# Kernel tuning notes

Hardware: AMD Instinct MI355X
Metric: run time of the kernel (lower is better)

Reference implementation:

```python
import jax, jax.numpy as jnp
import numpy as np

B, S, D = 4, 2048, 1024

def setup_inputs() -> dict:
    key = jax.random.key(0)
    kv, kk, kq, kw = jax.random.split(key, 4)
    scale = 1.0 / np.sqrt(D)
    v = jax.random.normal(kv, (B, S, D), dtype=jnp.float32)
    k = jax.random.normal(kk, (B, S, D), dtype=jnp.float32)
    q = jax.random.normal(kq, (B, S, D), dtype=jnp.float32)
    wi = jax.random.normal(kw, (D, D), dtype=jnp.float32) * scale
    mask = jnp.tril(jnp.ones((S, S), dtype=bool))[None, :, :]  # causal [1,S,S]
    return {"v": v, "k": k, "q": q, "wi": wi, "mask": mask}

def reference(v, k, q, wi, mask):
    # project q, k, v with the shared weight wi
    q = q @ wi
    k = k @ wi
    v = v @ wi
    # scaled dot-product scores [B,S,S]
    scores = jnp.einsum('bqd,bkd->bqk', q, k) / jnp.sqrt(jnp.asarray(q.shape[-1], q.dtype))
    scores = jnp.where(mask, scores, jnp.asarray(-1e10, scores.dtype))
    attn = jax.nn.softmax(scores, axis=-1)
    # residual: q + attn @ v
    return q + jnp.einsum('bqk,bkd->bqd', attn, v)
```

## Files before the change

### kernel.cpp

```cpp
#include <hip/hip_runtime.h>
#include <hip/hip_bf16.h>

typedef __hip_bfloat16 bf16;
typedef short bf16x8 __attribute__((ext_vector_type(8)));
typedef float f32x4 __attribute__((ext_vector_type(4)));

#define HT 16384

__device__ __forceinline__ void gload16(const void* g, void* l) {
    __builtin_amdgcn_global_load_lds(
        (const __attribute__((address_space(1))) void*)g,
        (__attribute__((address_space(3))) void*)l, 16, 0, 0);
}

__device__ __forceinline__ void stage_half(char* lds, const bf16* src, int ld,
                                           int rowbase, int k0, int slotIdx,
                                           int tid)
{
    char* dst = lds + (size_t)slotIdx * HT + tid * 16;
    const int sub = tid >> 3;
    const int cb  = ((tid & 7) ^ (sub & 7)) << 4;
    #pragma unroll
    for (int p = 0; p < 2; ++p) {
        const int row = p * 64 + sub;
        const char* g = (const char*)(src + (size_t)(rowbase + row) * ld + k0) + cb;
        gload16(g, dst + p * 8192);
    }
}

__device__ __forceinline__ void stage_q(char* lds, const bf16* src, int ld,
                                        int rowbase, int k0, int slotIdx,
                                        int tid)
{
    char* dst = lds + (size_t)slotIdx * HT + tid * 16;
    #pragma unroll
    for (int p = 0; p < 4; ++p) {
        const int s = p * 256 + tid;
        const int row = s >> 3;
        const int cb = ((s & 7) ^ (row & 7)) << 4;
        const char* g = (const char*)(src + (size_t)(rowbase + row) * ld + k0) + cb;
        gload16(g, dst + p * 4096);
    }
}

__device__ __forceinline__ bf16x8 ldsfrag(const char* lds, int slotIdx,
                                          int row, int ks, int cb0)
{
    return *(const bf16x8*)(lds + (size_t)slotIdx * HT
                            + row * 128 + (cb0 ^ (ks << 6)));
}

__device__ __forceinline__ float bf2f(short s) {
    union { float f; unsigned u; } c;
    c.u = ((unsigned)(unsigned short)s) << 16;
    return c.f;
}

#define MF8(n0)                                                               \
    _Pragma("unroll") for (int m = 0; m < 4; ++m)                             \
    _Pragma("unroll") for (int dn = 0; dn < 2; ++dn)                          \
    _Pragma("unroll") for (int ks = 0; ks < 2; ++ks)                          \
        acc[m][(n0)+dn] = __builtin_amdgcn_mfma_f32_16x16x32_bf16(            \
            af[m][ks], bv[(n0)+dn][ks], acc[m][(n0)+dn], 0, 0, 0);

#define GEMM256_BODY(A_, lda_, B_, ldb_, brow_, bcol_)                        \
    f32x4 acc[4][4] = {};                                                     \
    bf16x8 af[4][2], bv[4][2];                                                \
    stage_half(lds, A_, lda_, brow_,       0, 0, tid);                        \
    stage_half(lds, A_, lda_, brow_ + 128, 0, 1, tid);                        \
    stage_half(lds, B_, ldb_, bcol_,       0, 6, tid);                        \
    stage_half(lds, A_, lda_, brow_,      64, 2, tid);                        \
    stage_half(lds, A_, lda_, brow_ + 128,64, 3, tid);                        \
    stage_half(lds, B_, ldb_, bcol_,     64, 7, tid);                         \
    asm volatile("s_waitcnt vmcnt(6)" ::: "memory");                          \
    __builtin_amdgcn_s_barrier();                                             \
    for (int t = 0; t < 16; ++t) {                                            \
        const int aslot = (t % 3) * 2 + hA;                                   \
        const int bslot = 6 + (t & 1);                                        \
        const int a2    = ((t + 2) % 3) * 2;                                  \
        const int k2    = min(t + 2, 15) << 6;                                \
        _Pragma("unroll") for (int m = 0; m < 4; ++m)                         \
        _Pragma("unroll") for (int ks = 0; ks < 2; ++ks)                      \
            af[m][ks] = ldsfrag(lds, aslot, rA + m * 16 + fr, ks, cb0);       \
        _Pragma("unroll") for (int n = 0; n < 4; ++n)                         \
        _Pragma("unroll") for (int ks = 0; ks < 2; ++ks)                      \
            bv[n][ks] = ldsfrag(lds, bslot, rB + n * 16 + fr, ks, cb0);       \
        stage_half(lds, A_, lda_, brow_,       k2, a2,     tid);              \
        stage_half(lds, A_, lda_, brow_ + 128, k2, a2 + 1, tid);              \
        __builtin_amdgcn_s_barrier();                                         \
        __builtin_amdgcn_s_setprio(1);                                        \
        MF8(0)                                                                \
        __builtin_amdgcn_s_setprio(0);                                        \
        __builtin_amdgcn_s_barrier();                                         \
        stage_half(lds, B_, ldb_, bcol_, k2, bslot, tid);                     \
        __builtin_amdgcn_s_barrier();                                         \
        __builtin_amdgcn_s_setprio(1);                                        \
        MF8(2)                                                                \
        __builtin_amdgcn_s_setprio(0);                                        \
        asm volatile("s_waitcnt vmcnt(6)" ::: "memory");                      \
        __builtin_amdgcn_s_barrier();                                         \
    }

template<int MODE>
__launch_bounds__(512, 2)
__global__ void gemm_a256(const bf16* __restrict__ A, const bf16* __restrict__ B,
                          bf16* __restrict__ Cb, float* __restrict__ Cf)
{
    extern __shared__ char lds[];
    const int gx = gridDim.x;
    const int nwg = gx * gridDim.y;
    const int chunk = nwg >> 3;
    const int orig = blockIdx.y * gx + blockIdx.x;
    const int wk2 = (orig & 7) * chunk + (orig >> 3);
    const int bi = wk2 / gx, bj = wk2 % gx;
    const int brow = bi * 256, bcol = bj * 128;

    const int tid  = threadIdx.x;
    const int lane = tid & 63;
    const int w    = tid >> 6;
    const int wm   = w >> 1, wn = w & 1;
    const int fr   = lane & 15, fq = lane >> 4;
    const int cb0  = ((fr & 7) ^ fq) << 4;
    const int hA   = wm >> 1;
    const int rA   = (wm & 1) * 64;
    const int rB   = wn * 64;

    GEMM256_BODY(A, 1024, B, 1024, brow, bcol)

    #pragma unroll
    for (int mf = 0; mf < 4; ++mf) {
        const int r0 = brow + wm * 64 + mf * 16 + fq * 4;
        #pragma unroll
        for (int nf = 0; nf < 4; ++nf) {
            const int c = bcol + wn * 64 + nf * 16 + fr;
            #pragma unroll
            for (int j = 0; j < 4; ++j) {
                if (MODE == 0)
                    Cb[(size_t)(r0 + j) * 1024 + c] =
                        __float2bfloat16(acc[mf][nf][j]);
                else
                    Cf[(size_t)(r0 + j) * 1024 + c] = acc[mf][nf][j];
            }
        }
    }
}

__launch_bounds__(512, 1)
__global__ void scores8(const bf16* __restrict__ qG, const bf16* __restrict__ kb,
                        bf16* __restrict__ P)
{
    extern __shared__ char lds[];
    const int orig = blockIdx.y * 8 + blockIdx.x;
    const int wk2 = (orig & 7) * 18 + (orig >> 3);
    const int bz = wk2 / 36;
    const int j  = wk2 % 36;
    int bi = (int)((__fsqrt_rn(8.0f * j + 1.0f) - 1.0f) * 0.5f);
    while ((bi + 1) * (bi + 2) / 2 <= j) ++bi;
    while (bi * (bi + 1) / 2 > j) --bi;
    const int bj = j - bi * (bi + 1) / 2;
    const int brow = bi * 256, bcol = bj * 256;
    const bf16* A = qG + (size_t)bz * 2048 * 1024;
    const bf16* B = kb + (size_t)bz * 2048 * 1024;
    bf16* Cp = P + (size_t)bz * 2048 * 2048;

    const int tid  = threadIdx.x;
    const int lane = tid & 63;
    const int w    = tid >> 6;
    const int wm   = w >> 2;
    const int wn   = w & 3;
    const int bh   = wn >> 1;
    const int rBl  = (wn & 1) * 64;
    const int fr   = lane & 15, fq = lane >> 4;
    const int cb0  = ((fr & 7) ^ fq) << 4;

    f32x4 acc[8][4] = {};
    bf16x8 af0[4][2], af1[4][2], bv0[2][2], bv1[2][2];

#define AS(t,h) ((((t) % 3) * 2) + (h))
#define BS(t,h) (6 + (((t) & 1) * 2) + (h))

    stage_half(lds, A, 1024, brow,       0, AS(0,0), tid);
    stage_half(lds, A, 1024, brow + 128, 0, AS(0,1), tid);
    stage_half(lds, B, 1024, bcol,       0, BS(0,0), tid);
    stage_half(lds, B, 1024, bcol + 128, 0, BS(0,1), tid);
    stage_half(lds, A, 1024, brow,      64, AS(1,0), tid);
    stage_half(lds, A, 1024, brow + 128,64, AS(1,1), tid);
    stage_half(lds, B, 1024, bcol,     64, BS(1,0), tid);
    asm volatile("s_waitcnt vmcnt(6)" ::: "memory");
    __builtin_amdgcn_s_barrier();

#define MFQ(MH, NH, AF, BV)                                                   \
    _Pragma("unroll") for (int m = 0; m < 4; ++m)                             \
    _Pragma("unroll") for (int n = 0; n < 2; ++n)                             \
    _Pragma("unroll") for (int ks = 0; ks < 2; ++ks)                          \
        acc[(MH)*4+m][(NH)*2+n] = __builtin_amdgcn_mfma_f32_16x16x32_bf16(    \
            AF[m][ks], BV[n][ks], acc[(MH)*4+m][(NH)*2+n], 0, 0, 0);

    for (int t = 0; t < 16; ++t) {
        const int kN  = min(t + 1, 15) << 6;
        const int kNN = min(t + 2, 15) << 6;
        const int as  = AS(t, wm);
        const int bs2 = BS(t, bh);

        #pragma unroll
        for (int m = 0; m < 4; ++m)
            #pragma unroll
            for (int ks = 0; ks < 2; ++ks)
                af0[m][ks] = ldsfrag(lds, as, m * 16 + fr, ks, cb0);
        #pragma unroll
        for (int n = 0; n < 2; ++n)
            #pragma unroll
            for (int ks = 0; ks < 2; ++ks)
                bv0[n][ks] = ldsfrag(lds, bs2, rBl + n * 16 + fr, ks, cb0);
        stage_half(lds, B, 1024, bcol + 128, kN, BS(t + 1, 1), tid);
        __builtin_amdgcn_s_barrier();
        __builtin_amdgcn_s_setprio(1);
        MFQ(0, 0, af0, bv0)
        __builtin_amdgcn_s_setprio(0);
        __builtin_amdgcn_s_barrier();

        #pragma unroll
        for (int m = 0; m < 4; ++m)
            #pragma unroll
            for (int ks = 0; ks < 2; ++ks)
                af1[m][ks] = ldsfrag(lds, as, 64 + m * 16 + fr, ks, cb0);
        stage_half(lds, A, 1024, brow, kNN, AS(t + 2, 0), tid);
        __builtin_amdgcn_s_barrier();
        __builtin_amdgcn_s_setprio(1);
        MFQ(1, 0, af1, bv0)
        __builtin_amdgcn_s_setprio(0);
        __builtin_amdgcn_s_barrier();

        #pragma unroll
        for (int n = 0; n < 2; ++n)
            #pragma unroll
            for (int ks = 0; ks < 2; ++ks)
                bv1[n][ks] = ldsfrag(lds, bs2, rBl + 32 + n * 16 + fr, ks, cb0);
        stage_half(lds, A, 1024, brow + 128, kNN, AS(t + 2, 1), tid);
        __builtin_amdgcn_s_barrier();
        __builtin_amdgcn_s_setprio(1);
        MFQ(1, 1, af1, bv1)
        __builtin_amdgcn_s_setprio(0);
        __builtin_amdgcn_s_barrier();

        stage_half(lds, B, 1024, bcol, kNN, BS(t + 2, 0), tid);
        __builtin_amdgcn_s_barrier();
        __builtin_amdgcn_s_setprio(1);
        MFQ(0, 1, af0, bv1)
        __builtin_amdgcn_s_setprio(0);
        asm volatile("s_waitcnt vmcnt(6)" ::: "memory");
        __builtin_amdgcn_s_barrier();
    }
#undef MFQ
#undef AS
#undef BS

    #pragma unroll
    for (int mf = 0; mf < 8; ++mf) {
        const int r0 = brow + wm * 128 + mf * 16 + fq * 4;
        #pragma unroll
        for (int nf = 0; nf < 4; ++nf) {
            const int c = bcol + wn * 64 + nf * 16 + fr;
            #pragma unroll
            for (int jj = 0; jj < 4; ++jj)
                Cp[(size_t)(r0 + jj) * 2048 + c] =
                    __float2bfloat16(acc[mf][nf][jj] * 0.03125f);
        }
    }
}

__device__ __forceinline__ void tile128pv(char* lds, const bf16* A, const bf16* B,
                                          bf16* Cb, const bf16* Res,
                                          int lda, int ldb, int ldcb,
                                          int brow, int bcol, int NT, int tid)
{
    const int lane = tid & 63;
    const int w    = tid >> 6;
    const int wm   = w >> 1, wn = w & 1;
    const int fr   = lane & 15, fq = lane >> 4;
    const int cb0  = ((fr & 7) ^ fq) << 4;

    f32x4 acc[4][4] = {};
    bf16x8 af[4][2], bv[4][2];

    stage_q(lds, A, lda, brow, 0,  0, tid);
    stage_q(lds, B, ldb, bcol, 0,  3, tid);
    stage_q(lds, A, lda, brow, 64, 1, tid);
    stage_q(lds, B, ldb, bcol, 64, 4, tid);
    asm volatile("s_waitcnt vmcnt(8)" ::: "memory");
    __builtin_amdgcn_s_barrier();

    for (int t = 0; t < NT; ++t) {
        const int aslot = t % 3, bslot = 3 + (t & 1);
        const int k2 = min(t + 2, NT - 1) << 6;

        #pragma unroll
        for (int m = 0; m < 4; ++m)
            #pragma unroll
            for (int ks = 0; ks < 2; ++ks)
                af[m][ks] = ldsfrag(lds, aslot, wm * 64 + m * 16 + fr, ks, cb0);
        #pragma unroll
        for (int n = 0; n < 4; ++n)
            #pragma unroll
            for (int ks = 0; ks < 2; ++ks)
                bv[n][ks] = ldsfrag(lds, bslot, wn * 64 + n * 16 + fr, ks, cb0);
        stage_q(lds, A, lda, brow, k2, (t + 2) % 3, tid);
        __builtin_amdgcn_s_barrier();
        __builtin_amdgcn_s_setprio(1);
        #pragma unroll
        for (int m = 0; m < 4; ++m)
            #pragma unroll
            for (int n = 0; n < 2; ++n)
                #pragma unroll
                for (int ks = 0; ks < 2; ++ks)
                    acc[m][n] = __builtin_amdgcn_mfma_f32_16x16x32_bf16(
                        af[m][ks], bv[n][ks], acc[m][n], 0, 0, 0);
        __builtin_amdgcn_s_setprio(0);
        __builtin_amdgcn_s_barrier();

        stage_q(lds, B, ldb, bcol, k2, bslot, tid);
        __builtin_amdgcn_s_barrier();
        __builtin_amdgcn_s_setprio(1);
        #pragma unroll
        for (int m = 0; m < 4; ++m)
            #pragma unroll
            for (int n = 2; n < 4; ++n)
                #pragma unroll
                for (int ks = 0; ks < 2; ++ks)
                    acc[m][n] = __builtin_amdgcn_mfma_f32_16x16x32_bf16(
                        af[m][ks], bv[n][ks], acc[m][n], 0, 0, 0);
        __builtin_amdgcn_s_setprio(0);
        asm volatile("s_waitcnt vmcnt(8)" ::: "memory");
        __builtin_amdgcn_s_barrier();
    }

    #pragma unroll
    for (int mf = 0; mf < 4; ++mf) {
        const int r0 = brow + wm * 64 + mf * 16 + fq * 4;
        #pragma unroll
        for (int nf = 0; nf < 4; ++nf) {
            const int c = bcol + wn * 64 + nf * 16 + fr;
            #pragma unroll
            for (int j = 0; j < 4; ++j)
                Cb[(size_t)(r0 + j) * ldcb + c] = __float2bfloat16(
                    acc[mf][nf][j] +
                    __bfloat162float(Res[(size_t)(r0 + j) * ldcb + c]));
        }
    }
}

__launch_bounds__(256, 2)
__global__ void pv128(const bf16* __restrict__ P, const bf16* __restrict__ vT,
                      const bf16* __restrict__ qb, bf16* __restrict__ Y)
{
    extern __shared__ char lds[];
    const int x  = blockIdx.x;
    const int u  = x & 255;
    const int bs = u & 7;
    const int bj = (u >> 3) & 7;
    const int bz = u >> 6;
    const int bi = (x >> 8) ? (15 - bs) : bs;

    tile128pv(lds,
              P + (size_t)bz * 2048 * 2048,
              vT + (size_t)bz * 1024 * 2048,
              Y + (size_t)bz * 2048 * 1024,
              qb + (size_t)bz * 2048 * 1024,
              2048, 2048, 1024,
              bi * 128, bj * 128, 2 * (bi + 1), threadIdx.x);
}

__global__ void convert_qk_w(const float* __restrict__ q, const float* __restrict__ k,
                             const float* __restrict__ wi,
                             bf16* __restrict__ qb, bf16* __restrict__ kb,
                             bf16* __restrict__ Wb)
{
    const int N8 = 8192 * 1024 / 8;
    const int W8 = 1024 * 1024 / 8;
    const int total = 2 * N8 + W8;
    for (int i = blockIdx.x * 256 + threadIdx.x; i < total; i += gridDim.x * 256) {
        const float4* s;
        bf16* dst;
        int j;
        if (i < N8)            { s = (const float4*)q;  dst = qb; j = i; }
        else if (i < 2 * N8)   { s = (const float4*)k;  dst = kb; j = i - N8; }
        else                   { s = (const float4*)wi; dst = Wb; j = i - 2 * N8; }
        float4 a = s[2 * j], b = s[2 * j + 1];
        float vals[8] = {a.x, a.y, a.z, a.w, b.x, b.y, b.z, b.w};
        union { short h[8]; bf16x8 v8; } o;
        #pragma unroll
        for (int e = 0; e < 8; ++e) {
            bf16 hh = __float2bfloat16(vals[e]);
            o.h[e] = *(short*)&hh;
        }
        ((bf16x8*)dst)[j] = o.v8;
    }
}

__global__ void transpose_vwi(const float* __restrict__ v,
                              const float* __restrict__ wi,
                              bf16* __restrict__ vT, bf16* __restrict__ Wt)
{
    __shared__ float t[32][33];
    const int z = blockIdx.z;
    const int lx = threadIdx.x & 31, ly = threadIdx.x >> 5;
    if (z < 4) {
        const int d0 = blockIdx.x * 32, s0 = blockIdx.y * 32;
        const float* src = v + (size_t)z * 2048 * 1024;
        bf16* dst = vT + (size_t)z * 1024 * 2048;
        for (int i = ly; i < 32; i += 8)
            t[i][lx] = src[(size_t)(s0 + i) * 1024 + d0 + lx];
        __syncthreads();
        for (int i = ly; i < 32; i += 8)
            dst[(size_t)(d0 + i) * 2048 + s0 + lx] = __float2bfloat16(t[lx][i]);
    } else {
        if (blockIdx.y >= 32) return;
        const int n0 = blockIdx.x * 32, k0 = blockIdx.y * 32;
        for (int i = ly; i < 32; i += 8)
            t[i][lx] = wi[(size_t)(k0 + i) * 1024 + n0 + lx];
        __syncthreads();
        for (int i = ly; i < 32; i += 8)
            Wt[(size_t)(n0 + i) * 1024 + k0 + lx] = __float2bfloat16(t[lx][i]);
    }
}

__launch_bounds__(256)
__global__ void softmax_rows(bf16* __restrict__ P)
{
    const int wid = threadIdx.x >> 6, lane = threadIdx.x & 63;
    const int r = blockIdx.x * 4 + wid, b = blockIdx.y;
    bf16* row = P + ((size_t)b * 2048 + r) * 2048;
    const int nv  = r + 1;
    const int rup = (r & ~127) + 128;

    float vals[4][8];
    float m = -1e30f;
    #pragma unroll
    for (int c = 0; c < 4; ++c) {
        const int k0 = c * 512 + lane * 8;
        if (k0 < rup) {
            bf16x8 x = *(const bf16x8*)(row + k0);
            #pragma unroll
            for (int j = 0; j < 8; ++j) {
                float f = (k0 + j < nv) ? bf2f(x[j]) : -1e30f;
                vals[c][j] = f;
                m = fmaxf(m, f);
            }
        } else {
            #pragma unroll
            for (int j = 0; j < 8; ++j) vals[c][j] = -1e30f;
        }
    }
    #pragma unroll
    for (int o = 32; o; o >>= 1) m = fmaxf(m, __shfl_xor(m, o));

    float sum = 0.f;
    #pragma unroll
    for (int c = 0; c < 4; ++c)
        #pragma unroll
        for (int j = 0; j < 8; ++j) {
            float e = __expf(vals[c][j] - m);
            vals[c][j] = e;
            sum += e;
        }
    #pragma unroll
    for (int o = 32; o; o >>= 1) sum += __shfl_xor(sum, o);
    const float inv = 1.0f / sum;

    #pragma unroll
    for (int c = 0; c < 4; ++c) {
        const int k0 = c * 512 + lane * 8;
        if (k0 < rup) {
            union { short h[8]; bf16x8 v8; } o;
            #pragma unroll
            for (int j = 0; j < 8; ++j) {
                bf16 hh = __float2bfloat16(vals[c][j] * inv);
                o.h[j] = *(short*)&hh;
            }
            *(bf16x8*)(row + k0) = o.v8;
        }
    }
}

extern "C" void kernel_launch(void* const* d_in, const int* in_sizes, int n_in,
                              void* d_out, int out_size, void* d_ws, size_t ws_size,
                              hipStream_t stream)
{
    const float* v  = (const float*)d_in[0];
    const float* k  = (const float*)d_in[1];
    const float* q  = (const float*)d_in[2];
    const float* wi = (const float*)d_in[3];
    float* out = (float*)d_out;

    char* ws = (char*)d_ws;
    const size_t MB = 1u << 20;
    bf16* Wb = (bf16*)(ws);
    bf16* Wt = (bf16*)(ws + 2 * MB);
    bf16* G  = (bf16*)(ws + 4 * MB);
    bf16* qb = (bf16*)(ws + 6 * MB);
    bf16* kb = (bf16*)(ws + 22 * MB);
    bf16* vT = (bf16*)(ws + 38 * MB);
    bf16* qG = (bf16*)(ws + 54 * MB);
    bf16* Y  = (bf16*)(ws + 70 * MB);
    bf16* P  = (bf16*)(ws + 86 * MB);

    (void)hipFuncSetAttribute((const void*)gemm_a256<0>,
            hipFuncAttributeMaxDynamicSharedMemorySize, 131072);
    (void)hipFuncSetAttribute((const void*)gemm_a256<2>,
            hipFuncAttributeMaxDynamicSharedMemorySize, 131072);
    (void)hipFuncSetAttribute((const void*)scores8,
            hipFuncAttributeMaxDynamicSharedMemorySize, 163840);
    (void)hipFuncSetAttribute((const void*)pv128,
            hipFuncAttributeMaxDynamicSharedMemorySize, 81920);

    convert_qk_w<<<2048, 256, 0, stream>>>(q, k, wi, qb, kb, Wb);
    transpose_vwi<<<dim3(32, 64, 5), 256, 0, stream>>>(v, wi, vT, Wt);

    gemm_a256<0><<<dim3(8, 4), 512, 131072, stream>>>(Wb, Wb, G, nullptr);

    gemm_a256<0><<<dim3(8, 32), 512, 131072, stream>>>(qb, G, qG, nullptr);

    scores8<<<dim3(8, 18), 512, 163840, stream>>>(qG, kb, P);

    softmax_rows<<<dim3(512, 4), 256, 0, stream>>>(P);

    pv128<<<dim3(512), 256, 81920, stream>>>(P, vT, qb, Y);

    gemm_a256<2><<<dim3(8, 32), 512, 131072, stream>>>(Y, Wt, nullptr, out);
}
```

Before: 164.9 us.

## Fuse Gram, qG, scores and softmax into one cooperative persistent kernel

Merges the W·Wᵀ GEMM, the q·G projection, the causal score GEMM and the row softmax into a single cooperative kernel of 144 workgroups that separates phases with grid-wide syncs. The projection GEMMs now use the same 256x256 eight-phase tile routine as the score kernel. The conversion and transpose prep kernels are also merged into one launch. The aim is to remove launch gaps and tail effects between small dependent kernels. In exchange it adds grid-sync costs, leaves some workgroups idle in the early GEMM phases (16 and 128 of 144 tiles), and depends on cooperative launch co-residency.

```diff
diff --git a/kernel.cpp b/kernel.cpp
--- a/kernel.cpp
+++ b/kernel.cpp
@@ -1,5 +1,8 @@
 #include <hip/hip_runtime.h>
 #include <hip/hip_bf16.h>
+#include <hip/hip_cooperative_groups.h>
+
+namespace cg = cooperative_groups;
 
 typedef __hip_bfloat16 bf16;
 typedef short bf16x8 __attribute__((ext_vector_type(8)));
@@ -56,6 +59,318 @@
     return c.f;
 }
 
+__device__ __forceinline__ void tile256_8ph(char* lds,
+                                            const bf16* __restrict__ A,
+                                            const bf16* __restrict__ B,
+                                            bf16* __restrict__ C, int ldc,
+                                            int brow, int bcol, float scale,
+                                            int tid)
+{
+    const int lane = tid & 63;
+    const int w    = tid >> 6;
+    const int wm   = w >> 2;
+    const int wn   = w & 3;
+    const int bh   = wn >> 1;
+    const int rBl  = (wn & 1) * 64;
+    const int fr   = lane & 15, fq = lane >> 4;
+    const int cb0  = ((fr & 7) ^ fq) << 4;
+
+    f32x4 acc[8][4] = {};
+    bf16x8 af0[4][2], af1[4][2], bv0[2][2], bv1[2][2];
+
+#define AS(t,h) ((((t) % 3) * 2) + (h))
+#define BS(t,h) (6 + (((t) & 1) * 2) + (h))
+
+    stage_half(lds, A, 1024, brow,       0, AS(0,0), tid);
+    stage_half(lds, A, 1024, brow + 128, 0, AS(0,1), tid);
+    stage_half(lds, B, 1024, bcol,       0, BS(0,0), tid);
+    stage_half(lds, B, 1024, bcol + 128, 0, BS(0,1), tid);
+    stage_half(lds, A, 1024, brow,      64, AS(1,0), tid);
+    stage_half(lds, A, 1024, brow + 128,64, AS(1,1), tid);
+    stage_half(lds, B, 1024, bcol,     64, BS(1,0), tid);
+    asm volatile("s_waitcnt vmcnt(6)" ::: "memory");
+    __builtin_amdgcn_s_barrier();
+
+#define MFQ(MH, NH, AF, BV)                                                   \
+    _Pragma("unroll") for (int m = 0; m < 4; ++m)                             \
+    _Pragma("unroll") for (int n = 0; n < 2; ++n)                             \
+    _Pragma("unroll") for (int ks = 0; ks < 2; ++ks)                          \
+        acc[(MH)*4+m][(NH)*2+n] = __builtin_amdgcn_mfma_f32_16x16x32_bf16(    \
+            AF[m][ks], BV[n][ks], acc[(MH)*4+m][(NH)*2+n], 0, 0, 0);
+
+    for (int t = 0; t < 16; ++t) {
+        const int kN  = min(t + 1, 15) << 6;
+        const int kNN = min(t + 2, 15) << 6;
+        const int as  = AS(t, wm);
+        const int bs2 = BS(t, bh);
+
+        #pragma unroll
+        for (int m = 0; m < 4; ++m)
+            #pragma unroll
+            for (int ks = 0; ks < 2; ++ks)
+                af0[m][ks] = ldsfrag(lds, as, m * 16 + fr, ks, cb0);
+        #pragma unroll
+        for (int n = 0; n < 2; ++n)
+            #pragma unroll
+            for (int ks = 0; ks < 2; ++ks)
+                bv0[n][ks] = ldsfrag(lds, bs2, rBl + n * 16 + fr, ks, cb0);
+        stage_half(lds, B, 1024, bcol + 128, kN, BS(t + 1, 1), tid);
+        __builtin_amdgcn_s_barrier();
+        __builtin_amdgcn_s_setprio(1);
+        MFQ(0, 0, af0, bv0)
+        __builtin_amdgcn_s_setprio(0);
+        __builtin_amdgcn_s_barrier();
+
+        #pragma unroll
+        for (int m = 0; m < 4; ++m)
+            #pragma unroll
+            for (int ks = 0; ks < 2; ++ks)
+                af1[m][ks] = ldsfrag(lds, as, 64 + m * 16 + fr, ks, cb0);
+        stage_half(lds, A, 1024, brow, kNN, AS(t + 2, 0), tid);
+        __builtin_amdgcn_s_barrier();
+        __builtin_amdgcn_s_setprio(1);
+        MFQ(1, 0, af1, bv0)
+        __builtin_amdgcn_s_setprio(0);
+        __builtin_amdgcn_s_barrier();
+
+        #pragma unroll
+        for (int n = 0; n < 2; ++n)
+            #pragma unroll
+            for (int ks = 0; ks < 2; ++ks)
+                bv1[n][ks] = ldsfrag(lds, bs2, rBl + 32 + n * 16 + fr, ks, cb0);
+        stage_half(lds, A, 1024, brow + 128, kNN, AS(t + 2, 1), tid);
+        __builtin_amdgcn_s_barrier();
+        __builtin_amdgcn_s_setprio(1);
+        MFQ(1, 1, af1, bv1)
+        __builtin_amdgcn_s_setprio(0);
+        __builtin_amdgcn_s_barrier();
+
+        stage_half(lds, B, 1024, bcol, kNN, BS(t + 2, 0), tid);
+        __builtin_amdgcn_s_barrier();
+        __builtin_amdgcn_s_setprio(1);
+        MFQ(0, 1, af0, bv1)
+        __builtin_amdgcn_s_setprio(0);
+        asm volatile("s_waitcnt vmcnt(6)" ::: "memory");
+        __builtin_amdgcn_s_barrier();
+    }
+#undef MFQ
+#undef AS
+#undef BS
+
+    #pragma unroll
+    for (int mf = 0; mf < 8; ++mf) {
+        const int r0 = brow + wm * 128 + mf * 16 + fq * 4;
+        #pragma unroll
+        for (int nf = 0; nf < 4; ++nf) {
+            const int c = bcol + wn * 64 + nf * 16 + fr;
+            #pragma unroll
+            for (int jj = 0; jj < 4; ++jj)
+                C[(size_t)(r0 + jj) * ldc + c] =
+                    __float2bfloat16(acc[mf][nf][jj] * scale);
+        }
+    }
+    asm volatile("s_waitcnt vmcnt(0)" ::: "memory");
+    __builtin_amdgcn_s_barrier();
+}
+
+__launch_bounds__(512, 1)
+__global__ void attn_mega(const bf16* __restrict__ Wb,
+                          const bf16* __restrict__ qb,
+                          const bf16* __restrict__ kb,
+                          bf16* __restrict__ G, bf16* __restrict__ qG,
+                          bf16* __restrict__ P)
+{
+    extern __shared__ char lds[];
+    cg::grid_group grid = cg::this_grid();
+    const int orig = blockIdx.x;
+    const int wk2 = (orig & 7) * 18 + (orig >> 3);
+    const int tid = threadIdx.x;
+
+    if (wk2 < 16)
+        tile256_8ph(lds, Wb, Wb, G, 1024,
+                    (wk2 >> 2) * 256, (wk2 & 3) * 256, 1.0f, tid);
+    grid.sync();
+
+    if (wk2 < 128)
+        tile256_8ph(lds, qb, G, qG, 1024,
+                    (wk2 >> 2) * 256, (wk2 & 3) * 256, 1.0f, tid);
+    grid.sync();
+
+    {
+        const int bz = wk2 / 36;
+        const int j  = wk2 % 36;
+        int bi = (int)((__fsqrt_rn(8.0f * j + 1.0f) - 1.0f) * 0.5f);
+        while ((bi + 1) * (bi + 2) / 2 <= j) ++bi;
+        while (bi * (bi + 1) / 2 > j) --bi;
+        const int bj = j - bi * (bi + 1) / 2;
+        tile256_8ph(lds,
+                    qG + (size_t)bz * 2048 * 1024,
+                    kb + (size_t)bz * 2048 * 1024,
+                    P + (size_t)bz * 2048 * 2048, 2048,
+                    bi * 256, bj * 256, 0.03125f, tid);
+    }
+    grid.sync();
+
+    {
+        const int w = tid >> 6, lane = tid & 63;
+        for (int row = orig * 8 + w; row < 8192; row += 144 * 8) {
+            const int b = row >> 11, r = row & 2047;
+            bf16* rp = P + ((size_t)b * 2048 + r) * 2048;
+            const int nv  = r + 1;
+            const int rup = (r & ~127) + 128;
+
+            float vals[4][8];
+            float m = -1e30f;
+            #pragma unroll
+            for (int c = 0; c < 4; ++c) {
+                const int k0 = c * 512 + lane * 8;
+                if (k0 < rup) {
+                    bf16x8 x = *(const bf16x8*)(rp + k0);
+                    #pragma unroll
+                    for (int j = 0; j < 8; ++j) {
+                        float f = (k0 + j < nv) ? bf2f(x[j]) : -1e30f;
+                        vals[c][j] = f;
+                        m = fmaxf(m, f);
+                    }
+                } else {
+                    #pragma unroll
+                    for (int j = 0; j < 8; ++j) vals[c][j] = -1e30f;
+                }
+            }
+            #pragma unroll
+            for (int o = 32; o; o >>= 1) m = fmaxf(m, __shfl_xor(m, o));
+
+            float sum = 0.f;
+            #pragma unroll
+            for (int c = 0; c < 4; ++c)
+                #pragma unroll
+                for (int j = 0; j < 8; ++j) {
+                    float e = __expf(vals[c][j] - m);
+                    vals[c][j] = e;
+                    sum += e;
+                }
+            #pragma unroll
+            for (int o = 32; o; o >>= 1) sum += __shfl_xor(sum, o);
+            const float inv = 1.0f / sum;
+
+            #pragma unroll
+            for (int c = 0; c < 4; ++c) {
+                const int k0 = c * 512 + lane * 8;
+                if (k0 < rup) {
+                    union { short h[8]; bf16x8 v8; } o;
+                    #pragma unroll
+                    for (int j = 0; j < 8; ++j) {
+                        bf16 hh = __float2bfloat16(vals[c][j] * inv);
+                        o.h[j] = *(short*)&hh;
+                    }
+                    *(bf16x8*)(rp + k0) = o.v8;
+                }
+            }
+        }
+    }
+}
+
+__device__ __forceinline__ void tile128pv(char* lds, const bf16* A, const bf16* B,
+                                          bf16* Cb, const bf16* Res,
+                                          int lda, int ldb, int ldcb,
+                                          int brow, int bcol, int NT, int tid)
+{
+    const int lane = tid & 63;
+    const int w    = tid >> 6;
+    const int wm   = w >> 1, wn = w & 1;
+    const int fr   = lane & 15, fq = lane >> 4;
+    const int cb0  = ((fr & 7) ^ fq) << 4;
+
+    f32x4 acc[4][4] = {};
+    bf16x8 af[4][2], bv[4][2];
+
+    stage_q(lds, A, lda, brow, 0,  0, tid);
+    stage_q(lds, B, ldb, bcol, 0,  3, tid);
+    stage_q(lds, A, lda, brow, 64, 1, tid);
+    stage_q(lds, B, ldb, bcol, 64, 4, tid);
+    asm volatile("s_waitcnt vmcnt(8)" ::: "memory");
+    __builtin_amdgcn_s_barrier();
+
+    for (int t = 0; t < NT; ++t) {
+        const int aslot = t % 3, bslot = 3 + (t & 1);
+        const int k2 = min(t + 2, NT - 1) << 6;
+
+        #pragma unroll
+        for (int m = 0; m < 4; ++m)
+            #pragma unroll
+            for (int ks = 0; ks < 2; ++ks)
+                af[m][ks] = ldsfrag(lds, aslot, wm * 64 + m * 16 + fr, ks, cb0);
+        #pragma unroll
+        for (int n = 0; n < 4; ++n)
+            #pragma unroll
+            for (int ks = 0; ks < 2; ++ks)
+                bv[n][ks] = ldsfrag(lds, bslot, wn * 64 + n * 16 + fr, ks, cb0);
+        stage_q(lds, A, lda, brow, k2, (t + 2) % 3, tid);
+        __builtin_amdgcn_s_barrier();
+        __builtin_amdgcn_s_setprio(1);
+        #pragma unroll
+        for (int m = 0; m < 4; ++m)
+            #pragma unroll
+            for (int n = 0; n < 2; ++n)
+                #pragma unroll
+                for (int ks = 0; ks < 2; ++ks)
+                    acc[m][n] = __builtin_amdgcn_mfma_f32_16x16x32_bf16(
+                        af[m][ks], bv[n][ks], acc[m][n], 0, 0, 0);
+        __builtin_amdgcn_s_setprio(0);
+        __builtin_amdgcn_s_barrier();
+
+        stage_q(lds, B, ldb, bcol, k2, bslot, tid);
+        __builtin_amdgcn_s_barrier();
+        __builtin_amdgcn_s_setprio(1);
+        #pragma unroll
+        for (int m = 0; m < 4; ++m)
+            #pragma unroll
+            for (int n = 2; n < 4; ++n)
+                #pragma unroll
+                for (int ks = 0; ks < 2; ++ks)
+                    acc[m][n] = __builtin_amdgcn_mfma_f32_16x16x32_bf16(
+                        af[m][ks], bv[n][ks], acc[m][n], 0, 0, 0);
+        __builtin_amdgcn_s_setprio(0);
+        asm volatile("s_waitcnt vmcnt(8)" ::: "memory");
+        __builtin_amdgcn_s_barrier();
+    }
+
+    #pragma unroll
+    for (int mf = 0; mf < 4; ++mf) {
+        const int r0 = brow + wm * 64 + mf * 16 + fq * 4;
+        #pragma unroll
+        for (int nf = 0; nf < 4; ++nf) {
+            const int c = bcol + wn * 64 + nf * 16 + fr;
+            #pragma unroll
+            for (int j = 0; j < 4; ++j)
+                Cb[(size_t)(r0 + j) * ldcb + c] = __float2bfloat16(
+                    acc[mf][nf][j] +
+                    __bfloat162float(Res[(size_t)(r0 + j) * ldcb + c]));
+        }
+    }
+}
+
+__launch_bounds__(256, 2)
+__global__ void pv128(const bf16* __restrict__ P, const bf16* __restrict__ vT,
+                      const bf16* __restrict__ qb, bf16* __restrict__ Y)
+{
+    extern __shared__ char lds[];
+    const int x  = blockIdx.x;
+    const int u  = x & 255;
+    const int bs = u & 7;
+    const int bj = (u >> 3) & 7;
+    const int bz = u >> 6;
+    const int bi = (x >> 8) ? (15 - bs) : bs;
+
+    tile128pv(lds,
+              P + (size_t)bz * 2048 * 2048,
+              vT + (size_t)bz * 1024 * 2048,
+              Y + (size_t)bz * 2048 * 1024,
+              qb + (size_t)bz * 2048 * 1024,
+              2048, 2048, 1024,
+              bi * 128, bj * 128, 2 * (bi + 1), threadIdx.x);
+}
+
 #define MF8(n0)                                                               \
     _Pragma("unroll") for (int m = 0; m < 4; ++m)                             \
     _Pragma("unroll") for (int dn = 0; dn < 2; ++dn)                          \
@@ -63,48 +378,9 @@
         acc[m][(n0)+dn] = __builtin_amdgcn_mfma_f32_16x16x32_bf16(            \
             af[m][ks], bv[(n0)+dn][ks], acc[m][(n0)+dn], 0, 0, 0);
 
-#define GEMM256_BODY(A_, lda_, B_, ldb_, brow_, bcol_)                        \
-    f32x4 acc[4][4] = {};                                                     \
-    bf16x8 af[4][2], bv[4][2];                                                \
-    stage_half(lds, A_, lda_, brow_,       0, 0, tid);                        \
-    stage_half(lds, A_, lda_, brow_ + 128, 0, 1, tid);                        \
-    stage_half(lds, B_, ldb_, bcol_,       0, 6, tid);                        \
-    stage_half(lds, A_, lda_, brow_,      64, 2, tid);                        \
-    stage_half(lds, A_, lda_, brow_ + 128,64, 3, tid);                        \
-    stage_half(lds, B_, ldb_, bcol_,     64, 7, tid);                         \
-    asm volatile("s_waitcnt vmcnt(6)" ::: "memory");                          \
-    __builtin_amdgcn_s_barrier();                                             \
-    for (int t = 0; t < 16; ++t) {                                            \
-        const int aslot = (t % 3) * 2 + hA;                                   \
-        const int bslot = 6 + (t & 1);                                        \
-        const int a2    = ((t + 2) % 3) * 2;                                  \
-        const int k2    = min(t + 2, 15) << 6;                                \
-        _Pragma("unroll") for (int m = 0; m < 4; ++m)                         \
-        _Pragma("unroll") for (int ks = 0; ks < 2; ++ks)                      \
-            af[m][ks] = ldsfrag(lds, aslot, rA + m * 16 + fr, ks, cb0);       \
-        _Pragma("unroll") for (int n = 0; n < 4; ++n)                         \
-        _Pragma("unroll") for (int ks = 0; ks < 2; ++ks)                      \
-            bv[n][ks] = ldsfrag(lds, bslot, rB + n * 16 + fr, ks, cb0);       \
-        stage_half(lds, A_, lda_, brow_,       k2, a2,     tid);              \
-        stage_half(lds, A_, lda_, brow_ + 128, k2, a2 + 1, tid);              \
-        __builtin_amdgcn_s_barrier();                                         \
-        __builtin_amdgcn_s_setprio(1);                                        \
-        MF8(0)                                                                \
-        __builtin_amdgcn_s_setprio(0);                                        \
-        __builtin_amdgcn_s_barrier();                                         \
-        stage_half(lds, B_, ldb_, bcol_, k2, bslot, tid);                     \
-        __builtin_amdgcn_s_barrier();                                         \
-        __builtin_amdgcn_s_setprio(1);                                        \
-        MF8(2)                                                                \
-        __builtin_amdgcn_s_setprio(0);                                        \
-        asm volatile("s_waitcnt vmcnt(6)" ::: "memory");                      \
-        __builtin_amdgcn_s_barrier();                                         \
-    }
-
-template<int MODE>
 __launch_bounds__(512, 2)
-__global__ void gemm_a256(const bf16* __restrict__ A, const bf16* __restrict__ B,
-                          bf16* __restrict__ Cb, float* __restrict__ Cf)
+__global__ void final_gemm(const bf16* __restrict__ A, const bf16* __restrict__ B,
+                           float* __restrict__ Cf)
 {
     extern __shared__ char lds[];
     const int gx = gridDim.x;
@@ -125,7 +401,50 @@
     const int rA   = (wm & 1) * 64;
     const int rB   = wn * 64;
 
-    GEMM256_BODY(A, 1024, B, 1024, brow, bcol)
+    f32x4 acc[4][4] = {};
+    bf16x8 af[4][2], bv[4][2];
+
+    stage_half(lds, A, 1024, brow,       0, 0, tid);
+    stage_half(lds, A, 1024, brow + 128, 0, 1, tid);
+    stage_half(lds, B, 1024, bcol,       0, 6, tid);
+    stage_half(lds, A, 1024, brow,      64, 2, tid);
+    stage_half(lds, A, 1024, brow + 128,64, 3, tid);
+    stage_half(lds, B, 1024, bcol,     64, 7, tid);
+    asm volatile("s_waitcnt vmcnt(6)" ::: "memory");
+    __builtin_amdgcn_s_barrier();
+
+    for (int t = 0; t < 16; ++t) {
+        const int aslot = (t % 3) * 2 + hA;
+        const int bslot = 6 + (t & 1);
+        const int a2    = ((t + 2) % 3) * 2;
+        const int k2    = min(t + 2, 15) << 6;
+
+        #pragma unroll
+        for (int m = 0; m < 4; ++m)
+            #pragma unroll
+            for (int ks = 0; ks < 2; ++ks)
+                af[m][ks] = ldsfrag(lds, aslot, rA + m * 16 + fr, ks, cb0);
+        #pragma unroll
+        for (int n = 0; n < 4; ++n)
+            #pragma unroll
+            for (int ks = 0; ks < 2; ++ks)
+                bv[n][ks] = ldsfrag(lds, bslot, rB + n * 16 + fr, ks, cb0);
+        stage_half(lds, A, 1024, brow,       k2, a2,     tid);
+        stage_half(lds, A, 1024, brow + 128, k2, a2 + 1, tid);
+        __builtin_amdgcn_s_barrier();
+        __builtin_amdgcn_s_setprio(1);
+        MF8(0)
+        __builtin_amdgcn_s_setprio(0);
+        __builtin_amdgcn_s_barrier();
+
+        stage_half(lds, B, 1024, bcol, k2, bslot, tid);
+        __builtin_amdgcn_s_barrier();
+        __builtin_amdgcn_s_setprio(1);
+        MF8(2)
+        __builtin_amdgcn_s_setprio(0);
+        asm volatile("s_waitcnt vmcnt(6)" ::: "memory");
+        __builtin_amdgcn_s_barrier();
+    }
 
     #pragma unroll
     for (int mf = 0; mf < 4; ++mf) {
@@ -134,278 +453,24 @@
         for (int nf = 0; nf < 4; ++nf) {
             const int c = bcol + wn * 64 + nf * 16 + fr;
             #pragma unroll
-            for (int j = 0; j < 4; ++j) {
-                if (MODE == 0)
-                    Cb[(size_t)(r0 + j) * 1024 + c] =
-                        __float2bfloat16(acc[mf][nf][j]);
-                else
-                    Cf[(size_t)(r0 + j) * 1024 + c] = acc[mf][nf][j];
-            }
+            for (int j = 0; j < 4; ++j)
+                Cf[(size_t)(r0 + j) * 1024 + c] = acc[mf][nf][j];
         }
     }
 }
 
-__launch_bounds__(512, 1)
-__global__ void scores8(const bf16* __restrict__ qG, const bf16* __restrict__ kb,
-                        bf16* __restrict__ P)
-{
-    extern __shared__ char lds[];
-    const int orig = blockIdx.y * 8 + blockIdx.x;
-    const int wk2 = (orig & 7) * 18 + (orig >> 3);
-    const int bz = wk2 / 36;
-    const int j  = wk2 % 36;
-    int bi = (int)((__fsqrt_rn(8.0f * j + 1.0f) - 1.0f) * 0.5f);
-    while ((bi + 1) * (bi + 2) / 2 <= j) ++bi;
-    while (bi * (bi + 1) / 2 > j) --bi;
-    const int bj = j - bi * (bi + 1) / 2;
-    const int brow = bi * 256, bcol = bj * 256;
-    const bf16* A = qG + (size_t)bz * 2048 * 1024;
-    const bf16* B = kb + (size_t)bz * 2048 * 1024;
-    bf16* Cp = P + (size_t)bz * 2048 * 2048;
-
-    const int tid  = threadIdx.x;
-    const int lane = tid & 63;
-    const int w    = tid >> 6;
-    const int wm   = w >> 2;
-    const int wn   = w & 3;
-    const int bh   = wn >> 1;
-    const int rBl  = (wn & 1) * 64;
-    const int fr   = lane & 15, fq = lane >> 4;
-    const int cb0  = ((fr & 7) ^ fq) << 4;
-
-    f32x4 acc[8][4] = {};
-    bf16x8 af0[4][2], af1[4][2], bv0[2][2], bv1[2][2];
-
-#define AS(t,h) ((((t) % 3) * 2) + (h))
-#define BS(t,h) (6 + (((t) & 1) * 2) + (h))
-
-    stage_half(lds, A, 1024, brow,       0, AS(0,0), tid);
-    stage_half(lds, A, 1024, brow + 128, 0, AS(0,1), tid);
-    stage_half(lds, B, 1024, bcol,       0, BS(0,0), tid);
-    stage_half(lds, B, 1024, bcol + 128, 0, BS(0,1), tid);
-    stage_half(lds, A, 1024, brow,      64, AS(1,0), tid);
-    stage_half(lds, A, 1024, brow + 128,64, AS(1,1), tid);
-    stage_half(lds, B, 1024, bcol,     64, BS(1,0), tid);
-    asm volatile("s_waitcnt vmcnt(6)" ::: "memory");
-    __builtin_amdgcn_s_barrier();
-
-#define MFQ(MH, NH, AF, BV)                                                   \
-    _Pragma("unroll") for (int m = 0; m < 4; ++m)                             \
-    _Pragma("unroll") for (int n = 0; n < 2; ++n)                             \
-    _Pragma("unroll") for (int ks = 0; ks < 2; ++ks)                          \
-        acc[(MH)*4+m][(NH)*2+n] = __builtin_amdgcn_mfma_f32_16x16x32_bf16(    \
-            AF[m][ks], BV[n][ks], acc[(MH)*4+m][(NH)*2+n], 0, 0, 0);
-
-    for (int t = 0; t < 16; ++t) {
-        const int kN  = min(t + 1, 15) << 6;
-        const int kNN = min(t + 2, 15) << 6;
-        const int as  = AS(t, wm);
-        const int bs2 = BS(t, bh);
-
-        #pragma unroll
-        for (int m = 0; m < 4; ++m)
-            #pragma unroll
-            for (int ks = 0; ks < 2; ++ks)
-                af0[m][ks] = ldsfrag(lds, as, m * 16 + fr, ks, cb0);
-        #pragma unroll
-        for (int n = 0; n < 2; ++n)
-            #pragma unroll
-            for (int ks = 0; ks < 2; ++ks)
-                bv0[n][ks] = ldsfrag(lds, bs2, rBl + n * 16 + fr, ks, cb0);
-        stage_half(lds, B, 1024, bcol + 128, kN, BS(t + 1, 1), tid);
-        __builtin_amdgcn_s_barrier();
-        __builtin_amdgcn_s_setprio(1);
-        MFQ(0, 0, af0, bv0)
-        __builtin_amdgcn_s_setprio(0);
-        __builtin_amdgcn_s_barrier();
-
-        #pragma unroll
-        for (int m = 0; m < 4; ++m)
-            #pragma unroll
-            for (int ks = 0; ks < 2; ++ks)
-                af1[m][ks] = ldsfrag(lds, as, 64 + m * 16 + fr, ks, cb0);
-        stage_half(lds, A, 1024, brow, kNN, AS(t + 2, 0), tid);
-        __builtin_amdgcn_s_barrier();
-        __builtin_amdgcn_s_setprio(1);
-        MFQ(1, 0, af1, bv0)
-        __builtin_amdgcn_s_setprio(0);
-        __builtin_amdgcn_s_barrier();
-
-        #pragma unroll
-        for (int n = 0; n < 2; ++n)
-            #pragma unroll
-            for (int ks = 0; ks < 2; ++ks)
-                bv1[n][ks] = ldsfrag(lds, bs2, rBl + 32 + n * 16 + fr, ks, cb0);
-        stage_half(lds, A, 1024, brow + 128, kNN, AS(t + 2, 1), tid);
-        __builtin_amdgcn_s_barrier();
-        __builtin_amdgcn_s_setprio(1);
-        MFQ(1, 1, af1, bv1)
-        __builtin_amdgcn_s_setprio(0);
-        __builtin_amdgcn_s_barrier();
-
-        stage_half(lds, B, 1024, bcol, kNN, BS(t + 2, 0), tid);
-        __builtin_amdgcn_s_barrier();
-        __builtin_amdgcn_s_setprio(1);
-        MFQ(0, 1, af0, bv1)
-        __builtin_amdgcn_s_setprio(0);
-        asm volatile("s_waitcnt vmcnt(6)" ::: "memory");
-        __builtin_amdgcn_s_barrier();
-    }
-#undef MFQ
-#undef AS
-#undef BS
-
-    #pragma unroll
-    for (int mf = 0; mf < 8; ++mf) {
-        const int r0 = brow + wm * 128 + mf * 16 + fq * 4;
-        #pragma unroll
-        for (int nf = 0; nf < 4; ++nf) {
-            const int c = bcol + wn * 64 + nf * 16 + fr;
-            #pragma unroll
-            for (int jj = 0; jj < 4; ++jj)
-                Cp[(size_t)(r0 + jj) * 2048 + c] =
-                    __float2bfloat16(acc[mf][nf][jj] * 0.03125f);
-        }
-    }
-}
-
-__device__ __forceinline__ void tile128pv(char* lds, const bf16* A, const bf16* B,
-                                          bf16* Cb, const bf16* Res,
-                                          int lda, int ldb, int ldcb,
-                                          int brow, int bcol, int NT, int tid)
-{
-    const int lane = tid & 63;
-    const int w    = tid >> 6;
-    const int wm   = w >> 1, wn = w & 1;
-    const int fr   = lane & 15, fq = lane >> 4;
-    const int cb0  = ((fr & 7) ^ fq) << 4;
-
-    f32x4 acc[4][4] = {};
-    bf16x8 af[4][2], bv[4][2];
-
-    stage_q(lds, A, lda, brow, 0,  0, tid);
-    stage_q(lds, B, ldb, bcol, 0,  3, tid);
-    stage_q(lds, A, lda, brow, 64, 1, tid);
-    stage_q(lds, B, ldb, bcol, 64, 4, tid);
-    asm volatile("s_waitcnt vmcnt(8)" ::: "memory");
-    __builtin_amdgcn_s_barrier();
-
-    for (int t = 0; t < NT; ++t) {
-        const int aslot = t % 3, bslot = 3 + (t & 1);
-        const int k2 = min(t + 2, NT - 1) << 6;
-
-        #pragma unroll
-        for (int m = 0; m < 4; ++m)
-            #pragma unroll
-            for (int ks = 0; ks < 2; ++ks)
-                af[m][ks] = ldsfrag(lds, aslot, wm * 64 + m * 16 + fr, ks, cb0);
-        #pragma unroll
-        for (int n = 0; n < 4; ++n)
-            #pragma unroll
-            for (int ks = 0; ks < 2; ++ks)
-                bv[n][ks] = ldsfrag(lds, bslot, wn * 64 + n * 16 + fr, ks, cb0);
-        stage_q(lds, A, lda, brow, k2, (t + 2) % 3, tid);
-        __builtin_amdgcn_s_barrier();
-        __builtin_amdgcn_s_setprio(1);
-        #pragma unroll
-        for (int m = 0; m < 4; ++m)
-            #pragma unroll
-            for (int n = 0; n < 2; ++n)
-                #pragma unroll
-                for (int ks = 0; ks < 2; ++ks)
-                    acc[m][n] = __builtin_amdgcn_mfma_f32_16x16x32_bf16(
-                        af[m][ks], bv[n][ks], acc[m][n], 0, 0, 0);
-        __builtin_amdgcn_s_setprio(0);
-        __builtin_amdgcn_s_barrier();
-
-        stage_q(lds, B, ldb, bcol, k2, bslot, tid);
-        __builtin_amdgcn_s_barrier();
-        __builtin_amdgcn_s_setprio(1);
-        #pragma unroll
-        for (int m = 0; m < 4; ++m)
-            #pragma unroll
-            for (int n = 2; n < 4; ++n)
-                #pragma unroll
-                for (int ks = 0; ks < 2; ++ks)
-                    acc[m][n] = __builtin_amdgcn_mfma_f32_16x16x32_bf16(
-                        af[m][ks], bv[n][ks], acc[m][n], 0, 0, 0);
-        __builtin_amdgcn_s_setprio(0);
-        asm volatile("s_waitcnt vmcnt(8)" ::: "memory");
-        __builtin_amdgcn_s_barrier();
-    }
-
-    #pragma unroll
-    for (int mf = 0; mf < 4; ++mf) {
-        const int r0 = brow + wm * 64 + mf * 16 + fq * 4;
-        #pragma unroll
-        for (int nf = 0; nf < 4; ++nf) {
-            const int c = bcol + wn * 64 + nf * 16 + fr;
-            #pragma unroll
-            for (int j = 0; j < 4; ++j)
-                Cb[(size_t)(r0 + j) * ldcb + c] = __float2bfloat16(
-                    acc[mf][nf][j] +
-                    __bfloat162float(Res[(size_t)(r0 + j) * ldcb + c]));
-        }
-    }
-}
-
-__launch_bounds__(256, 2)
-__global__ void pv128(const bf16* __restrict__ P, const bf16* __restrict__ vT,
-                      const bf16* __restrict__ qb, bf16* __restrict__ Y)
-{
-    extern __shared__ char lds[];
-    const int x  = blockIdx.x;
-    const int u  = x & 255;
-    const int bs = u & 7;
-    const int bj = (u >> 3) & 7;
-    const int bz = u >> 6;
-    const int bi = (x >> 8) ? (15 - bs) : bs;
-
-    tile128pv(lds,
-              P + (size_t)bz * 2048 * 2048,
-              vT + (size_t)bz * 1024 * 2048,
-              Y + (size_t)bz * 2048 * 1024,
-              qb + (size_t)bz * 2048 * 1024,
-              2048, 2048, 1024,
-              bi * 128, bj * 128, 2 * (bi + 1), threadIdx.x);
-}
-
-__global__ void convert_qk_w(const float* __restrict__ q, const float* __restrict__ k,
-                             const float* __restrict__ wi,
-                             bf16* __restrict__ qb, bf16* __restrict__ kb,
-                             bf16* __restrict__ Wb)
-{
-    const int N8 = 8192 * 1024 / 8;
-    const int W8 = 1024 * 1024 / 8;
-    const int total = 2 * N8 + W8;
-    for (int i = blockIdx.x * 256 + threadIdx.x; i < total; i += gridDim.x * 256) {
-        const float4* s;
-        bf16* dst;
-        int j;
-        if (i < N8)            { s = (const float4*)q;  dst = qb; j = i; }
-        else if (i < 2 * N8)   { s = (const float4*)k;  dst = kb; j = i - N8; }
-        else                   { s = (const float4*)wi; dst = Wb; j = i - 2 * N8; }
-        float4 a = s[2 * j], b = s[2 * j + 1];
-        float vals[8] = {a.x, a.y, a.z, a.w, b.x, b.y, b.z, b.w};
-        union { short h[8]; bf16x8 v8; } o;
-        #pragma unroll
-        for (int e = 0; e < 8; ++e) {
-            bf16 hh = __float2bfloat16(vals[e]);
-            o.h[e] = *(short*)&hh;
-        }
-        ((bf16x8*)dst)[j] = o.v8;
-    }
-}
-
-__global__ void transpose_vwi(const float* __restrict__ v,
-                              const float* __restrict__ wi,
-                              bf16* __restrict__ vT, bf16* __restrict__ Wt)
+__global__ void prep(const float* __restrict__ q, const float* __restrict__ k,
+                     const float* __restrict__ wi, const float* __restrict__ v,
+                     bf16* __restrict__ qb, bf16* __restrict__ kb,
+                     bf16* __restrict__ Wb, bf16* __restrict__ vT,
+                     bf16* __restrict__ Wt)
 {
     __shared__ float t[32][33];
-    const int z = blockIdx.z;
+    const int b = blockIdx.x;
     const int lx = threadIdx.x & 31, ly = threadIdx.x >> 5;
-    if (z < 4) {
-        const int d0 = blockIdx.x * 32, s0 = blockIdx.y * 32;
+    if (b < 8192) {
+        const int z = b >> 11, rem = b & 2047;
+        const int d0 = (rem & 31) * 32, s0 = (rem >> 5) * 32;
         const float* src = v + (size_t)z * 2048 * 1024;
         bf16* dst = vT + (size_t)z * 1024 * 2048;
         for (int i = ly; i < 32; i += 8)
@@ -413,71 +478,34 @@
         __syncthreads();
         for (int i = ly; i < 32; i += 8)
             dst[(size_t)(d0 + i) * 2048 + s0 + lx] = __float2bfloat16(t[lx][i]);
-    } else {
-        if (blockIdx.y >= 32) return;
-        const int n0 = blockIdx.x * 32, k0 = blockIdx.y * 32;
+    } else if (b < 9216) {
+        const int t2 = b - 8192;
+        const int n0 = (t2 & 31) * 32, k0 = (t2 >> 5) * 32;
         for (int i = ly; i < 32; i += 8)
             t[i][lx] = wi[(size_t)(k0 + i) * 1024 + n0 + lx];
         __syncthreads();
         for (int i = ly; i < 32; i += 8)
             Wt[(size_t)(n0 + i) * 1024 + k0 + lx] = __float2bfloat16(t[lx][i]);
-    }
-}
-
-__launch_bounds__(256)
-__global__ void softmax_rows(bf16* __restrict__ P)
-{
-    const int wid = threadIdx.x >> 6, lane = threadIdx.x & 63;
-    const int r = blockIdx.x * 4 + wid, b = blockIdx.y;
-    bf16* row = P + ((size_t)b * 2048 + r) * 2048;
-    const int nv  = r + 1;
-    const int rup = (r & ~127) + 128;
-
-    float vals[4][8];
-    float m = -1e30f;
-    #pragma unroll
-    for (int c = 0; c < 4; ++c) {
-        const int k0 = c * 512 + lane * 8;
-        if (k0 < rup) {
-            bf16x8 x = *(const bf16x8*)(row + k0);
-            #pragma unroll
-            for (int j = 0; j < 8; ++j) {
-                float f = (k0 + j < nv) ? bf2f(x[j]) : -1e30f;
-                vals[c][j] = f;
-                m = fmaxf(m, f);
+    } else {
+        const int N8 = 8192 * 1024 / 8, W8 = 1024 * 1024 / 8;
+        const int total = 2 * N8 + W8;
+        for (int i = (b - 9216) * 256 + threadIdx.x; i < total;
+             i += 3072 * 256) {
+            const float4* s;
+            bf16* dst;
+            int j;
+            if (i < N8)          { s = (const float4*)q;  dst = qb; j = i; }
+            else if (i < 2 * N8) { s = (const float4*)k;  dst = kb; j = i - N8; }
+            else                 { s = (const float4*)wi; dst = Wb; j = i - 2 * N8; }
+            float4 a = s[2 * j], bb = s[2 * j + 1];
+            float vals[8] = {a.x, a.y, a.z, a.w, bb.x, bb.y, bb.z, bb.w};
+            union { short h[8]; bf16x8 v8; } o;
+            #pragma unroll
+            for (int e = 0; e < 8; ++e) {
+                bf16 hh = __float2bfloat16(vals[e]);
+                o.h[e] = *(short*)&hh;
             }
-        } else {
-            #pragma unroll
-            for (int j = 0; j < 8; ++j) vals[c][j] = -1e30f;
-        }
-    }
-    #pragma unroll
-    for (int o = 32; o; o >>= 1) m = fmaxf(m, __shfl_xor(m, o));
-
-    float sum = 0.f;
-    #pragma unroll
-    for (int c = 0; c < 4; ++c)
-        #pragma unroll
-        for (int j = 0; j < 8; ++j) {
-            float e = __expf(vals[c][j] - m);
-            vals[c][j] = e;
-            sum += e;
-        }
-    #pragma unroll
-    for (int o = 32; o; o >>= 1) sum += __shfl_xor(sum, o);
-    const float inv = 1.0f / sum;
-
-    #pragma unroll
-    for (int c = 0; c < 4; ++c) {
-        const int k0 = c * 512 + lane * 8;
-        if (k0 < rup) {
-            union { short h[8]; bf16x8 v8; } o;
-            #pragma unroll
-            for (int j = 0; j < 8; ++j) {
-                bf16 hh = __float2bfloat16(vals[c][j] * inv);
-                o.h[j] = *(short*)&hh;
-            }
-            *(bf16x8*)(row + k0) = o.v8;
+            ((bf16x8*)dst)[j] = o.v8;
         }
     }
 }
@@ -504,27 +532,25 @@
     bf16* Y  = (bf16*)(ws + 70 * MB);
     bf16* P  = (bf16*)(ws + 86 * MB);
 
-    (void)hipFuncSetAttribute((const void*)gemm_a256<0>,
-            hipFuncAttributeMaxDynamicSharedMemorySize, 131072);
-    (void)hipFuncSetAttribute((const void*)gemm_a256<2>,
-            hipFuncAttributeMaxDynamicSharedMemorySize, 131072);
-    (void)hipFuncSetAttribute((const void*)scores8,
+    (void)hipFuncSetAttribute((const void*)attn_mega,
             hipFuncAttributeMaxDynamicSharedMemorySize, 163840);
     (void)hipFuncSetAttribute((const void*)pv128,
             hipFuncAttributeMaxDynamicSharedMemorySize, 81920);
-
-    convert_qk_w<<<2048, 256, 0, stream>>>(q, k, wi, qb, kb, Wb);
-    transpose_vwi<<<dim3(32, 64, 5), 256, 0, stream>>>(v, wi, vT, Wt);
-
-    gemm_a256<0><<<dim3(8, 4), 512, 131072, stream>>>(Wb, Wb, G, nullptr);
-
-    gemm_a256<0><<<dim3(8, 32), 512, 131072, stream>>>(qb, G, qG, nullptr);
-
-    scores8<<<dim3(8, 18), 512, 163840, stream>>>(qG, kb, P);
-
-    softmax_rows<<<dim3(512, 4), 256, 0, stream>>>(P);
+    (void)hipFuncSetAttribute((const void*)final_gemm,
+            hipFuncAttributeMaxDynamicSharedMemorySize, 131072);
+
+    prep<<<12288, 256, 0, stream>>>(q, k, wi, v, qb, kb, Wb, vT, Wt);
+
+    {
+        const bf16* Wb_ = Wb; const bf16* qb_ = qb; const bf16* kb_ = kb;
+        bf16* G_ = G; bf16* qG_ = qG; bf16* P_ = P;
+        void* args[] = {(void*)&Wb_, (void*)&qb_, (void*)&kb_,
+                        (void*)&G_, (void*)&qG_, (void*)&P_};
+        (void)hipLaunchCooperativeKernel((const void*)attn_mega,
+                dim3(144), dim3(512), args, 163840, stream);
+    }
 
     pv128<<<dim3(512), 256, 81920, stream>>>(P, vT, qb, Y);
 
-    gemm_a256<2><<<dim3(8, 32), 512, 131072, stream>>>(Y, Wt, nullptr, out);
-}
+    final_gemm<<<dim3(8, 32), 512, 131072, stream>>>(Y, Wt, out);
+}
```

Result: slower. 251.7 us (+52.6%).
